# Performance work log

Hardware: AMD Instinct MI355X
Metric: run time of the kernel (lower is better)

The kernel has to match this reference:

```python
import jax, jax.numpy as jnp
import numpy as np

B, S, D, H, F, PD = 2, 2048, 768, 12, 3072, 64


def layer_norm(x, w, b, eps=1e-5):
    m = jnp.mean(x, axis=-1, keepdims=True)
    v = jnp.var(x, axis=-1, keepdims=True)
    return (x - m) / jnp.sqrt(v + eps) * w + b


def setup_inputs() -> dict:
    key = jax.random.key(0)
    ks = jax.random.split(key, 8)
    sc = 0.02
    return {
        "x": jax.random.normal(ks[0], (B, S, D), jnp.float32),
        "ln1_w": jnp.ones((D,), jnp.float32),
        "ln1_b": jnp.zeros((D,), jnp.float32),
        "in_proj_w": jax.random.normal(ks[1], (3 * D, D), jnp.float32) * sc,
        "in_proj_b": jnp.zeros((3 * D,), jnp.float32),
        "phase_w": jax.random.normal(ks[2], (PD, D), jnp.float32) * sc,
        "alpha": jnp.float32(0.5),
        "ff_w1": jax.random.normal(ks[3], (F, D), jnp.float32) * sc,
        "ff_b1": jnp.zeros((F,), jnp.float32),
        "ff_w2": jax.random.normal(ks[4], (D, F), jnp.float32) * sc,
        "ff_b2": jnp.zeros((D,), jnp.float32),
        "ln2_w": jnp.ones((D,), jnp.float32),
        "ln2_b": jnp.zeros((D,), jnp.float32),
    }


def reference(x, ln1_w, ln1_b, in_proj_w, in_proj_b, phase_w, alpha,
              ff_w1, ff_b1, ff_w2, ff_b2, ln2_w, ln2_b):
    Dh = D // H
    xn = layer_norm(x, ln1_w, ln1_b)
    # MultiheadAttention with need_weights=True: only the head-averaged
    # softmax(QK^T/sqrt(Dh)) weights are consumed downstream (attn_out is
    # discarded in the original forward, so V/out_proj are dead code).
    qkv = xn @ in_proj_w.T + in_proj_b                       # [B,S,3D]
    q, k, _ = jnp.split(qkv, 3, axis=-1)
    q = q.reshape(B, S, H, Dh) * (1.0 / np.sqrt(Dh)).astype(np.float32)
    k = k.reshape(B, S, H, Dh)
    scores = jnp.einsum('bqhd,bkhd->bhqk', q, k)             # [B,H,S,S]
    attn_w = jax.nn.softmax(scores, axis=-1).mean(axis=1)    # head-avg [B,S,S]
    phase = jnp.tanh(xn @ phase_w.T)                         # [B,S,64]
    phase_coh = (phase @ phase.swapaxes(-2, -1) + 1.0) * 0.5  # [B,S,S]
    blended = jax.nn.softmax(jnp.log(attn_w + 1e-6) + alpha * phase_coh, axis=-1)
    x = x + blended @ xn                                     # enhanced context
    x2 = layer_norm(x, ln2_w, ln2_b)
    h = jax.nn.gelu(x2 @ ff_w1.T + ff_b1, approximate=False)  # exact GELU (torch default)
    ff = h @ ff_w2.T + ff_b2
    return x + ff
```

## Files before the change

### kernel.cpp

```cpp
#include <hip/hip_runtime.h>
#include <math.h>

typedef unsigned short u16;
typedef short bf8 __attribute__((ext_vector_type(8)));
typedef float f4 __attribute__((ext_vector_type(4)));

#define LOG2E 1.44269504088896340736f

__device__ __forceinline__ u16 f2b(float f) {
  union { float f; unsigned int u; } v; v.f = f;
  unsigned int u = v.u;
  return (u16)((u + 0x7FFFu + ((u >> 16) & 1u)) >> 16);
}
__device__ __forceinline__ float b2f(u16 u) {
  union { unsigned int i; float f; } v; v.i = ((unsigned int)u) << 16; return v.f;
}
__device__ __forceinline__ float ex2(float x) {
#if __has_builtin(__builtin_amdgcn_exp2f)
  return __builtin_amdgcn_exp2f(x);
#else
  return exp2f(x);
#endif
}
__device__ __forceinline__ float rcp_f(float x) {
#if __has_builtin(__builtin_amdgcn_rcpf)
  return __builtin_amdgcn_rcpf(x);
#else
  return 1.0f / x;
#endif
}
__device__ __forceinline__ float fast_tanh(float y) {
  return 1.0f - 2.0f * rcp_f(ex2(y * (2.0f * LOG2E)) + 1.0f);
}
__device__ __forceinline__ float fast_gelu(float v) {
  const float u = v * (0.79788456080286536f + 0.03567740814f * v * v);
  return 0.5f * v * (1.0f + fast_tanh(u));
}

template <int N>
__device__ __forceinline__ void waitvm() {
  if constexpr (N == 0)      asm volatile("s_waitcnt vmcnt(0)" ::: "memory");
  else if constexpr (N == 4) asm volatile("s_waitcnt vmcnt(4)" ::: "memory");
  else if constexpr (N == 6) asm volatile("s_waitcnt vmcnt(6)" ::: "memory");
  else if constexpr (N == 8) asm volatile("s_waitcnt vmcnt(8)" ::: "memory");
}

#define GLOAD_LDS16(gp, lp)                                                          \
  __builtin_amdgcn_global_load_lds(                                                  \
      reinterpret_cast<const __attribute__((address_space(1))) unsigned int*>(       \
          reinterpret_cast<uintptr_t>(gp)),                                          \
      reinterpret_cast<__attribute__((address_space(3))) unsigned int*>(             \
          reinterpret_cast<uintptr_t>(lp)),                                          \
      16, 0, 0)

template <int ISSUES>
__device__ __forceinline__ void stage_sw(const u16* gbase, long ldg, u16* lds,
                                         int wv, int lane) {
#pragma unroll
  for (int is = 0; is < ISSUES; ++is) {
    const int idx = is * 256 + wv * 64 + lane;
    const int r = idx >> 3, cs = idx & 7;
    const u16* gp = gbase + (long)r * ldg + ((cs ^ (r & 7)) << 3);
    GLOAD_LDS16(gp, (char*)lds + is * 4096 + wv * 1024);
  }
}
__device__ __forceinline__ bf8 frag_sw(const u16* lds, int r, int c) {
  return *(const bf8*)((const char*)lds + r * 128 + ((c ^ (r & 7)) << 4));
}

__global__ __launch_bounds__(256) void conv_bf16_k(const float* __restrict__ in,
                                                   u16* __restrict__ out, int n4) {
  int i = blockIdx.x * 256 + threadIdx.x;
  if (i >= n4) return;
  float4 v = ((const float4*)in)[i];
  union { u16 s[4]; uint2 u; } o;
  o.s[0] = f2b(v.x); o.s[1] = f2b(v.y); o.s[2] = f2b(v.z); o.s[3] = f2b(v.w);
  ((uint2*)out)[i] = o.u;
}

__global__ __launch_bounds__(256) void ln_bf16_k(const float* __restrict__ in,
                                                 const float* __restrict__ w,
                                                 const float* __restrict__ b,
                                                 u16* __restrict__ out) {
  const long row = blockIdx.x;
  const float* xr = in + row * 768;
  const int t = threadIdx.x;
  float v[3];
  float s = 0.f, q = 0.f;
#pragma unroll
  for (int i = 0; i < 3; ++i) {
    v[i] = xr[t + 256 * i];
    s += v[i]; q += v[i] * v[i];
  }
#pragma unroll
  for (int off = 1; off < 64; off <<= 1) { s += __shfl_xor(s, off); q += __shfl_xor(q, off); }
  __shared__ float rs[4], rq[4];
  const int wave = t >> 6, lane = t & 63;
  if (lane == 0) { rs[wave] = s; rq[wave] = q; }
  __syncthreads();
  s = rs[0] + rs[1] + rs[2] + rs[3];
  q = rq[0] + rq[1] + rq[2] + rq[3];
  const float mean = s * (1.0f / 768.0f);
  const float var = q * (1.0f / 768.0f) - mean * mean;
  const float rstd = rsqrtf(var + 1e-5f);
  u16* orow = out + row * 768;
#pragma unroll
  for (int i = 0; i < 3; ++i) {
    const int c = t + 256 * i;
    orow[c] = f2b((v[i] - mean) * rstd * w[c] + b[c]);
  }
}

__global__ __launch_bounds__(256) void transp_k(const u16* __restrict__ in,
                                                u16* __restrict__ out,
                                                float* __restrict__ rsum) {
  const int d0 = blockIdx.x * 64, s0 = blockIdx.y * 64;
  const int t = threadIdx.x;
  {
    const int bid = blockIdx.x + 12 * blockIdx.y;
    if (bid < 16) rsum[bid * 256 + t] = 0.f;
  }
  __shared__ u16 T[64][72];
  {
    const int r = t >> 3, c8 = (t & 7) * 8;
#pragma unroll
    for (int p = 0; p < 2; ++p) {
      const int rr = r + 32 * p;
      *(uint4*)&T[rr][c8] = *(const uint4*)&in[(long)(s0 + rr) * 768 + d0 + c8];
    }
  }
  __syncthreads();
  {
    const int d = t >> 3, s8 = (t & 7) * 8;
#pragma unroll
    for (int p = 0; p < 2; ++p) {
      const int dd = d + 32 * p;
      u16 tmp[8];
#pragma unroll
      for (int e = 0; e < 8; ++e) tmp[e] = T[s8 + e][dd];
      *(uint4*)&out[(long)(d0 + dd) * 4096 + s0 + s8] = *(uint4*)tmp;
    }
  }
}

template <int EPI, int TM>
__global__ __launch_bounds__(256) void mgemm5_k(
    const u16* __restrict__ A, int lda, long sA,
    const u16* __restrict__ B, int ldb, long sB,
    const float* __restrict__ bias,
    const float* __restrict__ res, long sR,
    void* __restrict__ O0, long sO, void* __restrict__ O1, void* __restrict__ O2,
    const int M, const int N, const int K) {
  constexpr int WR = (TM == 128) ? 2 : 1;
  constexpr int WC = 4 / WR;
  constexpr int MR = TM / (WR * 16);
  constexpr int NR = 128 / (WC * 16);
  constexpr int AISS = TM / 32;
  constexpr int BISS = 4;
  constexpr int NS = AISS + BISS;
  constexpr int AW = TM * 64;
  constexpr int BW = 128 * 64;
  __shared__ u16 As[2 * AW];
  __shared__ u16 Bs[2 * BW];
  const int t = threadIdx.x;
  const int wv = t >> 6, lane = t & 63;
  const int lr = lane & 15, lg = lane >> 4;
  const int wr = wv / WC, wc = wv % WC;
  const int wrow0 = wr * (MR * 16), wcol0 = wc * (NR * 16);

  const int gx = gridDim.x, gy = gridDim.y;
  const int nwg = gx * gy;
  const int cpx = nwg >> 3;
  const int flat = blockIdx.x + gx * blockIdx.y;
  const int nf = (flat & 7) * cpx + (flat >> 3);
  constexpr int G = 8;
  const int npg = G * gy;
  const int grp = nf / npg;
  const int firstn = grp * G;
  const int gsz = (gx - firstn < G) ? (gx - firstn) : G;
  const int rem = nf - grp * npg;
  const int m0 = (rem / gsz) * TM;
  const int n0 = (firstn + rem % gsz) * 128;

  const int bz = blockIdx.z;
  const u16* Ab = A + (long)bz * sA + (long)m0 * lda;
  const u16* Bb = B + (long)bz * sB + (long)n0 * ldb;
  const long zR = (long)bz * sR, zO = (long)bz * sO;

  const u16* ga[AISS];
  const u16* gb[BISS];
#pragma unroll
  for (int is = 0; is < AISS; ++is) {
    const int idx = is * 256 + wv * 64 + lane;
    const int r = idx >> 3, cs = idx & 7;
    ga[is] = Ab + (long)r * lda + ((cs ^ (r & 7)) << 3);
  }
#pragma unroll
  for (int is = 0; is < BISS; ++is) {
    const int idx = is * 256 + wv * 64 + lane;
    const int r = idx >> 3, cs = idx & 7;
    gb[is] = Bb + (long)r * ldb + ((cs ^ (r & 7)) << 3);
  }

  int offA[2][MR], offB[2][NR];
#pragma unroll
  for (int i = 0; i < MR; ++i) {
    const int r = wrow0 + i * 16 + lr;
    offA[0][i] = r * 128 + ((lg ^ (r & 7)) << 4);
    offA[1][i] = r * 128 + (((4 + lg) ^ (r & 7)) << 4);
  }
#pragma unroll
  for (int j = 0; j < NR; ++j) {
    const int r = wcol0 + j * 16 + lr;
    offB[0][j] = r * 128 + ((lg ^ (r & 7)) << 4);
    offB[1][j] = r * 128 + (((4 + lg) ^ (r & 7)) << 4);
  }

  f4 acc[MR][NR];
  const f4 fz = {0.f, 0.f, 0.f, 0.f};
#pragma unroll
  for (int i = 0; i < MR; ++i)
#pragma unroll
    for (int j = 0; j < NR; ++j) acc[i][j] = fz;

#pragma unroll
  for (int is = 0; is < AISS; ++is) {
    GLOAD_LDS16(ga[is], (char*)As + is * 4096 + wv * 1024);
    ga[is] += 64;
  }
#pragma unroll
  for (int is = 0; is < BISS; ++is) {
    GLOAD_LDS16(gb[is], (char*)Bs + is * 4096 + wv * 1024);
    gb[is] += 64;
  }

  const int NT = K >> 6;
  int cur = 0;
  for (int kt = 0; kt < NT; ++kt) {
    if (kt + 1 < NT) {
      char* bufA = (char*)(As + (cur ^ 1) * AW);
      char* bufB = (char*)(Bs + (cur ^ 1) * BW);
#pragma unroll
      for (int is = 0; is < AISS; ++is) {
        GLOAD_LDS16(ga[is], bufA + is * 4096 + wv * 1024);
        ga[is] += 64;
      }
#pragma unroll
      for (int is = 0; is < BISS; ++is) {
        GLOAD_LDS16(gb[is], bufB + is * 4096 + wv * 1024);
        gb[is] += 64;
      }
      waitvm<NS>();
    } else {
      waitvm<0>();
    }
    __builtin_amdgcn_s_barrier();
    const char* a = (const char*)(As + cur * AW);
    const char* b = (const char*)(Bs + cur * BW);
    bf8 af[2][MR], bf[2][NR];
#pragma unroll
    for (int s = 0; s < 2; ++s) {
#pragma unroll
      for (int i = 0; i < MR; ++i) af[s][i] = *(const bf8*)(a + offA[s][i]);
#pragma unroll
      for (int j = 0; j < NR; ++j) bf[s][j] = *(const bf8*)(b + offB[s][j]);
    }
#pragma unroll
    for (int s = 0; s < 2; ++s)
#pragma unroll
      for (int i = 0; i < MR; ++i)
#pragma unroll
        for (int j = 0; j < NR; ++j)
          acc[i][j] = __builtin_amdgcn_mfma_f32_16x16x32_bf16(af[s][i], bf[s][j], acc[i][j], 0, 0, 0);
    __builtin_amdgcn_s_barrier();
    cur ^= 1;
  }

#pragma unroll
  for (int i = 0; i < MR; ++i) {
    const int gr0 = m0 + wrow0 + i * 16 + lg * 4;
#pragma unroll
    for (int j = 0; j < NR; ++j) {
      const int gc = n0 + wcol0 + j * 16 + lr;
#pragma unroll
      for (int r = 0; r < 4; ++r) {
        const long row = gr0 + r;
        float v = acc[i][j][r];
        if (EPI == 0) {
          if (gc < 1536) {
            v += bias[gc];
            if (gc < 768) ((u16*)O0)[row * 768 + gc] = f2b(v * (0.125f * LOG2E));
            else          ((u16*)O1)[row * 768 + gc - 768] = f2b(v);
          } else if (gc < 1600) {
            ((u16*)O2)[row * 64 + gc - 1536] = f2b(fast_tanh(v));
          }
        } else if (EPI == 3) {
          ((u16*)O0)[row * N + gc] = f2b(fast_gelu(v + bias[gc]));
        } else if (EPI == 4) {
          ((float*)O0)[row * N + gc] = v + bias[gc] + res[row * N + gc];
        } else {
          const float sc = rcp_f(bias[(long)bz * M + row]);
          ((float*)O0)[zO + row * N + gc] = v * sc + res[zR + row * N + gc];
        }
      }
    }
  }
}

__global__ __launch_bounds__(256) void attn_stats4(const u16* __restrict__ qb,
                                                   const u16* __restrict__ kb,
                                                   float* __restrict__ Ms_g) {
  const int bid = blockIdx.x;
  const int s8 = bid & 7, idx = bid >> 3;
  const int qt = idx & 31;
  const int combo = s8 * 3 + (idx >> 5);
  const int h = combo % 12, b = combo / 12;
  const int t = threadIdx.x, wv = t >> 6, lane = t & 63;
  const int lr = lane & 15, lg = lane >> 4;
  __shared__ u16 Qs[64 * 64];
  __shared__ u16 Ks[2][128 * 64];
  __shared__ float zbuf[4][64];
  const long q0 = (long)b * 2048 + qt * 64;
  const long kbase = ((long)b * 2048) * 768 + h * 64;
  stage_sw<2>(qb + q0 * 768 + h * 64, 768, Qs, wv, lane);
  stage_sw<4>(kb + kbase, 768, Ks[0], wv, lane);
  waitvm<4>();
  __builtin_amdgcn_s_barrier();

  bf8 aq[4][2];
#pragma unroll
  for (int i = 0; i < 4; ++i)
#pragma unroll
    for (int kk = 0; kk < 2; ++kk)
      aq[i][kk] = frag_sw(Qs, i * 16 + lr, kk * 4 + lg);

  float zp[4][4];
#pragma unroll
  for (int i = 0; i < 4; ++i)
#pragma unroll
    for (int r = 0; r < 4; ++r) zp[i][r] = 0.f;

  const f4 fz = {0.f, 0.f, 0.f, 0.f};
  int cur = 0;
  for (int kt = 0; kt < 16; ++kt) {
    if (kt < 15) {
      stage_sw<4>(kb + kbase + (long)(kt + 1) * 128 * 768, 768, Ks[cur ^ 1], wv, lane);
      waitvm<4>();
    } else {
      waitvm<0>();
    }
    __builtin_amdgcn_s_barrier();
#pragma unroll
    for (int j = 0; j < 2; ++j) {
      const int krow = wv * 32 + j * 16 + lr;
      const bf8 b0 = frag_sw(Ks[cur], krow, lg);
      const bf8 b1 = frag_sw(Ks[cur], krow, 4 + lg);
#pragma unroll
      for (int i = 0; i < 4; ++i) {
        f4 s = fz;
        s = __builtin_amdgcn_mfma_f32_16x16x32_bf16(aq[i][0], b0, s, 0, 0, 0);
        s = __builtin_amdgcn_mfma_f32_16x16x32_bf16(aq[i][1], b1, s, 0, 0, 0);
#pragma unroll
        for (int r = 0; r < 4; ++r) zp[i][r] += ex2(s[r]);
      }
    }
    __builtin_amdgcn_s_barrier();
    cur ^= 1;
  }
#pragma unroll
  for (int i = 0; i < 4; ++i)
#pragma unroll
    for (int r = 0; r < 4; ++r) {
      float z = zp[i][r];
      z += __shfl_xor(z, 1); z += __shfl_xor(z, 2);
      z += __shfl_xor(z, 4); z += __shfl_xor(z, 8);
      zp[i][r] = z;
    }
  if (lr == 0) {
#pragma unroll
    for (int i = 0; i < 4; ++i)
#pragma unroll
      for (int r = 0; r < 4; ++r)
        zbuf[wv][i * 16 + lg * 4 + r] = zp[i][r];
  }
  __syncthreads();
  if (t < 64) {
    const float Z = zbuf[0][t] + zbuf[1][t] + zbuf[2][t] + zbuf[3][t];
    Ms_g[((long)(b * 12 + h)) * 2048 + qt * 64 + t] = log2f(12.0f * Z);
  }
}

__global__ __launch_bounds__(256) void blendpre10(const u16* __restrict__ qb,
                                                  const u16* __restrict__ kb,
                                                  const u16* __restrict__ ph,
                                                  const float* __restrict__ Ms_g,
                                                  const float* __restrict__ alpha_p,
                                                  u16* __restrict__ eb,
                                                  float* __restrict__ rsum) {
  const int bid = blockIdx.x;
  const int s8 = bid & 7, idx = bid >> 3;
  const int kt = ((s8 & 1) << 3) | (idx & 7);
  const int qt = (((s8 >> 1) & 1) << 3) | (idx >> 3);
  const int b = s8 >> 2;
  const int t = threadIdx.x, wv = t >> 6, lane = t & 63;
  const int lr = lane & 15, lg = lane >> 4;
  const int wr = wv >> 1, wc = wv & 1;
  const int q0 = qt * 128, k0 = kt * 128;
  __shared__ u16 Qs[2][128 * 64];
  __shared__ u16 Ks[2][128 * 64];
  __shared__ float Ms[12][128];
  for (int i2 = t; i2 < 1536; i2 += 256)
    Ms[i2 >> 7][i2 & 127] = Ms_g[((long)(b * 12 + (i2 >> 7))) * 2048 + q0 + (i2 & 127)];
  asm volatile("s_waitcnt vmcnt(0) lgkmcnt(0)" ::: "memory");
  __builtin_amdgcn_s_barrier();
  const float a2 = alpha_p[0] * 0.5f * LOG2E;

  f4 acc[4][4];
  const f4 fz = {0.f, 0.f, 0.f, 0.f};
#pragma unroll
  for (int i = 0; i < 4; ++i)
#pragma unroll
    for (int j = 0; j < 4; ++j) acc[i][j] = fz;

  const long qrow0 = (long)b * 2048 + q0;
  const long krow0 = (long)b * 2048 + k0;

  stage_sw<4>(qb + qrow0 * 768, 768, Qs[0], wv, lane);
  stage_sw<4>(kb + krow0 * 768, 768, Ks[0], wv, lane);

  int cur = 0;
  for (int h = 0; h < 12; ++h) {
    if (h < 11) {
      stage_sw<4>(qb + qrow0 * 768 + (h + 1) * 64, 768, Qs[cur ^ 1], wv, lane);
      stage_sw<4>(kb + krow0 * 768 + (h + 1) * 64, 768, Ks[cur ^ 1], wv, lane);
      waitvm<8>();
    } else {
      waitvm<0>();
    }
    __builtin_amdgcn_s_barrier();
    bf8 aq0[4], aq1[4], bk0[4], bk1[4];
#pragma unroll
    for (int i = 0; i < 4; ++i) {
      aq0[i] = frag_sw(Qs[cur], wr * 64 + i * 16 + lr, lg);
      aq1[i] = frag_sw(Qs[cur], wr * 64 + i * 16 + lr, 4 + lg);
    }
#pragma unroll
    for (int j = 0; j < 4; ++j) {
      bk0[j] = frag_sw(Ks[cur], wc * 64 + j * 16 + lr, lg);
      bk1[j] = frag_sw(Ks[cur], wc * 64 + j * 16 + lr, 4 + lg);
    }
#pragma unroll
    for (int i = 0; i < 4; ++i) {
      const f4 mv = *(const f4*)&Ms[h][wr * 64 + i * 16 + lg * 4];
      const f4 cin = fz - mv;
#pragma unroll
      for (int j = 0; j < 4; ++j) {
        f4 s = __builtin_amdgcn_mfma_f32_16x16x32_bf16(aq0[i], bk0[j], cin, 0, 0, 0);
        s = __builtin_amdgcn_mfma_f32_16x16x32_bf16(aq1[i], bk1[j], s, 0, 0, 0);
#pragma unroll
        for (int r = 0; r < 4; ++r) acc[i][j][r] += ex2(s[r]);
      }
    }
    __builtin_amdgcn_s_barrier();
    cur ^= 1;
  }

  float rs[4][4];
#pragma unroll
  for (int i = 0; i < 4; ++i)
#pragma unroll
    for (int r = 0; r < 4; ++r) rs[i][r] = 0.f;

#pragma unroll
  for (int i = 0; i < 4; ++i) {
    const u16* pa = ph + (qrow0 + wr * 64 + i * 16 + lr) * 64;
    const bf8 pa0 = *(const bf8*)(pa + lg * 8);
    const bf8 pa1 = *(const bf8*)(pa + 32 + lg * 8);
#pragma unroll
    for (int j = 0; j < 4; ++j) {
      const u16* pb = ph + (krow0 + wc * 64 + j * 16 + lr) * 64;
      const bf8 pb0 = *(const bf8*)(pb + lg * 8);
      const bf8 pb1 = *(const bf8*)(pb + 32 + lg * 8);
      f4 coh = fz;
      coh = __builtin_amdgcn_mfma_f32_16x16x32_bf16(pa0, pb0, coh, 0, 0, 0);
      coh = __builtin_amdgcn_mfma_f32_16x16x32_bf16(pa1, pb1, coh, 0, 0, 0);
#pragma unroll
      for (int r = 0; r < 4; ++r) {
        const long row = qrow0 + wr * 64 + i * 16 + lg * 4 + r;
        const int col = k0 + wc * 64 + j * 16 + lr;
        const float e = (acc[i][j][r] + 1e-6f) * ex2(a2 * (coh[r] + 1.0f));
        eb[row * 2048 + col] = f2b(e);
        rs[i][r] += e;
      }
    }
  }
#pragma unroll
  for (int i = 0; i < 4; ++i)
#pragma unroll
    for (int r = 0; r < 4; ++r) {
      float v = rs[i][r];
      v += __shfl_xor(v, 1); v += __shfl_xor(v, 2);
      v += __shfl_xor(v, 4); v += __shfl_xor(v, 8);
      if (lr == 0)
        atomicAdd(&rsum[qrow0 + wr * 64 + i * 16 + lg * 4 + r], v);
    }
}

extern "C" void kernel_launch(void* const* d_in, const int* in_sizes, int n_in,
                              void* d_out, int out_size, void* d_ws, size_t ws_size,
                              hipStream_t stream) {
  (void)in_sizes; (void)n_in; (void)out_size; (void)ws_size;
  const float* x         = (const float*)d_in[0];
  const float* ln1_w     = (const float*)d_in[1];
  const float* ln1_b     = (const float*)d_in[2];
  const float* in_proj_w = (const float*)d_in[3];
  const float* in_proj_b = (const float*)d_in[4];
  const float* phase_w   = (const float*)d_in[5];
  const float* alpha_p   = (const float*)d_in[6];
  const float* ff_w1     = (const float*)d_in[7];
  const float* ff_b1     = (const float*)d_in[8];
  const float* ff_w2     = (const float*)d_in[9];
  const float* ff_b2     = (const float*)d_in[10];
  const float* ln2_w     = (const float*)d_in[11];
  const float* ln2_b     = (const float*)d_in[12];
  float* out = (float*)d_out;

  char* w = (char*)d_ws;
  u16*   xn_b  = (u16*)w;            w += 6291456;
  u16*   xnT_b = (u16*)w;            w += 6291456;
  u16*   ph_b  = (u16*)w;            w += 524288;
  float* Ms_g  = (float*)w;          w += 196608;
  float* xmid  = (float*)w;          w += 12582912;
  char* big = w;
  u16* q_b  = (u16*)big;
  u16* k_b  = (u16*)(big + 6291456);
  u16* eb_b = (u16*)(big + 12582912);
  char* tail = big + 12582912 + 16777216;
  u16* wcat_b = (u16*)tail;
  float* rsum = (float*)(tail + 2555904);
  u16* h_b  = (u16*)big;
  char* wtail = tail + 16777216;
  u16* wff1_b = (u16*)wtail;
  u16* wff2_b = (u16*)(wtail + 4718592);
  u16* x2n_b = xn_b;

  conv_bf16_k<<<(1536 * 768 / 4 + 255) / 256, 256, 0, stream>>>(in_proj_w, wcat_b, 1536 * 768 / 4);
  conv_bf16_k<<<(64 * 768 / 4 + 255) / 256, 256, 0, stream>>>(phase_w, wcat_b + 1536 * 768, 64 * 768 / 4);
  conv_bf16_k<<<(3072 * 768 / 4 + 255) / 256, 256, 0, stream>>>(ff_w1, wff1_b, 3072 * 768 / 4);
  conv_bf16_k<<<(768 * 3072 / 4 + 255) / 256, 256, 0, stream>>>(ff_w2, wff2_b, 768 * 3072 / 4);

  ln_bf16_k<<<4096, 256, 0, stream>>>(x, ln1_w, ln1_b, xn_b);

  mgemm5_k<0, 128><<<dim3(13, 32, 1), 256, 0, stream>>>(
      xn_b, 768, 0, wcat_b, 768, 0, in_proj_b, nullptr, 0,
      q_b, 0, k_b, ph_b, 4096, 1664, 768);

  transp_k<<<dim3(12, 64), 256, 0, stream>>>(xn_b, xnT_b, rsum);

  attn_stats4<<<768, 256, 0, stream>>>(q_b, k_b, Ms_g);

  blendpre10<<<512, 256, 0, stream>>>(q_b, k_b, ph_b, Ms_g, alpha_p, eb_b, rsum);

  mgemm5_k<5, 64><<<dim3(6, 32, 2), 256, 0, stream>>>(
      eb_b, 2048, 2048L * 2048, xnT_b, 4096, 2048, rsum, x, 2048L * 768,
      xmid, 2048L * 768, nullptr, nullptr, 2048, 768, 2048);

  ln_bf16_k<<<4096, 256, 0, stream>>>(xmid, ln2_w, ln2_b, x2n_b);

  mgemm5_k<3, 128><<<dim3(24, 32, 1), 256, 0, stream>>>(
      x2n_b, 768, 0, wff1_b, 768, 0, ff_b1, nullptr, 0,
      h_b, 0, nullptr, nullptr, 4096, 3072, 768);

  mgemm5_k<4, 64><<<dim3(6, 64, 1), 256, 0, stream>>>(
      h_b, 3072, 0, wff2_b, 3072, 0, ff_b2, xmid, 0,
      out, 0, nullptr, nullptr, 4096, 768, 3072);
}
```

Baseline: 197.6 us.

## Replace double-buffered LDS GEMM pipeline with single buffer and register prefetch

```diff
diff --git a/kernel.cpp b/kernel.cpp
--- a/kernel.cpp
+++ b/kernel.cpp
@@ -144,7 +144,7 @@
 }
 
 template <int EPI, int TM>
-__global__ __launch_bounds__(256) void mgemm5_k(
+__global__ __launch_bounds__(256) void mgemm7_k(
     const u16* __restrict__ A, int lda, long sA,
     const u16* __restrict__ B, int ldb, long sB,
     const float* __restrict__ bias,
@@ -157,11 +157,8 @@
   constexpr int NR = 128 / (WC * 16);
   constexpr int AISS = TM / 32;
   constexpr int BISS = 4;
-  constexpr int NS = AISS + BISS;
-  constexpr int AW = TM * 64;
-  constexpr int BW = 128 * 64;
-  __shared__ u16 As[2 * AW];
-  __shared__ u16 Bs[2 * BW];
+  __shared__ u16 As[TM * 64];
+  __shared__ u16 Bs[128 * 64];
   const int t = threadIdx.x;
   const int wv = t >> 6, lane = t & 63;
   const int lr = lane & 15, lg = lane >> 4;
@@ -233,37 +230,33 @@
     GLOAD_LDS16(gb[is], (char*)Bs + is * 4096 + wv * 1024);
     gb[is] += 64;
   }
+  asm volatile("s_waitcnt vmcnt(0)" ::: "memory");
+  __builtin_amdgcn_s_barrier();
 
   const int NT = K >> 6;
-  int cur = 0;
   for (int kt = 0; kt < NT; ++kt) {
+    bf8 af[2][MR], bf[2][NR];
+#pragma unroll
+    for (int s = 0; s < 2; ++s) {
+#pragma unroll
+      for (int i = 0; i < MR; ++i) af[s][i] = *(const bf8*)((const char*)As + offA[s][i]);
+#pragma unroll
+      for (int j = 0; j < NR; ++j) bf[s][j] = *(const bf8*)((const char*)Bs + offB[s][j]);
+    }
+    asm volatile("s_waitcnt lgkmcnt(0)" ::: "memory");
+    __builtin_amdgcn_sched_barrier(0);
+    __builtin_amdgcn_s_barrier();
     if (kt + 1 < NT) {
-      char* bufA = (char*)(As + (cur ^ 1) * AW);
-      char* bufB = (char*)(Bs + (cur ^ 1) * BW);
 #pragma unroll
       for (int is = 0; is < AISS; ++is) {
-        GLOAD_LDS16(ga[is], bufA + is * 4096 + wv * 1024);
+        GLOAD_LDS16(ga[is], (char*)As + is * 4096 + wv * 1024);
         ga[is] += 64;
       }
 #pragma unroll
       for (int is = 0; is < BISS; ++is) {
-        GLOAD_LDS16(gb[is], bufB + is * 4096 + wv * 1024);
+        GLOAD_LDS16(gb[is], (char*)Bs + is * 4096 + wv * 1024);
         gb[is] += 64;
       }
-      waitvm<NS>();
-    } else {
-      waitvm<0>();
-    }
-    __builtin_amdgcn_s_barrier();
-    const char* a = (const char*)(As + cur * AW);
-    const char* b = (const char*)(Bs + cur * BW);
-    bf8 af[2][MR], bf[2][NR];
-#pragma unroll
-    for (int s = 0; s < 2; ++s) {
-#pragma unroll
-      for (int i = 0; i < MR; ++i) af[s][i] = *(const bf8*)(a + offA[s][i]);
-#pragma unroll
-      for (int j = 0; j < NR; ++j) bf[s][j] = *(const bf8*)(b + offB[s][j]);
     }
 #pragma unroll
     for (int s = 0; s < 2; ++s)
@@ -272,8 +265,8 @@
 #pragma unroll
         for (int j = 0; j < NR; ++j)
           acc[i][j] = __builtin_amdgcn_mfma_f32_16x16x32_bf16(af[s][i], bf[s][j], acc[i][j], 0, 0, 0);
+    asm volatile("s_waitcnt vmcnt(0)" ::: "memory");
     __builtin_amdgcn_s_barrier();
-    cur ^= 1;
   }
 
 #pragma unroll
@@ -551,7 +544,7 @@
 
   ln_bf16_k<<<4096, 256, 0, stream>>>(x, ln1_w, ln1_b, xn_b);
 
-  mgemm5_k<0, 128><<<dim3(13, 32, 1), 256, 0, stream>>>(
+  mgemm7_k<0, 128><<<dim3(13, 32, 1), 256, 0, stream>>>(
       xn_b, 768, 0, wcat_b, 768, 0, in_proj_b, nullptr, 0,
       q_b, 0, k_b, ph_b, 4096, 1664, 768);
 
@@ -561,17 +554,17 @@
 
   blendpre10<<<512, 256, 0, stream>>>(q_b, k_b, ph_b, Ms_g, alpha_p, eb_b, rsum);
 
-  mgemm5_k<5, 64><<<dim3(6, 32, 2), 256, 0, stream>>>(
+  mgemm7_k<5, 64><<<dim3(6, 32, 2), 256, 0, stream>>>(
       eb_b, 2048, 2048L * 2048, xnT_b, 4096, 2048, rsum, x, 2048L * 768,
       xmid, 2048L * 768, nullptr, nullptr, 2048, 768, 2048);
 
   ln_bf16_k<<<4096, 256, 0, stream>>>(xmid, ln2_w, ln2_b, x2n_b);
 
-  mgemm5_k<3, 128><<<dim3(24, 32, 1), 256, 0, stream>>>(
+  mgemm7_k<3, 128><<<dim3(24, 32, 1), 256, 0, stream>>>(
       x2n_b, 768, 0, wff1_b, 768, 0, ff_b1, nullptr, 0,
       h_b, 0, nullptr, nullptr, 4096, 3072, 768);
 
-  mgemm5_k<4, 64><<<dim3(6, 64, 1), 256, 0, stream>>>(
+  mgemm7_k<4, 64><<<dim3(6, 64, 1), 256, 0, stream>>>(
       h_b, 3072, 0, wff2_b, 3072, 0, ff_b2, xmid, 0,
       out, 0, nullptr, nullptr, 4096, 768, 3072);
 }
```

Measured after the change: 215.5 us. 9.1% more time.
